# Optimization experiments

Hardware: AMD Instinct MI355X
Metric: run time of the kernel (lower is better)

The kernel has to match this reference:

```python
import jax, jax.numpy as jnp
import numpy as np

N, E, W, G = 100000, 625000, 128, 64  # nodes, edges, width, num graphs
EPS = 1e-5


def setup_inputs() -> dict:
    key = jax.random.key(0)
    ks = jax.random.split(key, 8)
    x = jax.random.normal(ks[0], (N, W), jnp.float32)
    edge_index = jax.random.randint(ks[1], (2, E), 0, N, dtype=jnp.int32)
    edge_weight = jax.random.uniform(ks[2], (E,), jnp.float32)
    batch_map = jnp.sort(jax.random.randint(ks[3], (N,), 0, G, dtype=jnp.int32))
    s = 1.0 / np.sqrt(W)
    return {
        "x": x,
        "edge_index": edge_index,
        "edge_weight": edge_weight,
        "batch_map": batch_map,
        "gn_weight": jnp.ones((W,), jnp.float32),
        "gn_bias": jnp.zeros((W,), jnp.float32),
        "gn_mean_scale": jnp.ones((W,), jnp.float32),
        "W_rel1": jax.random.normal(ks[4], (W, W), jnp.float32) * s,
        "b_rel1": jnp.zeros((W,), jnp.float32),
        "W_root1": jax.random.normal(ks[5], (W, W), jnp.float32) * s,
        "W_rel2": jax.random.normal(ks[6], (W, W), jnp.float32) * s,
        "b_rel2": jnp.zeros((W,), jnp.float32),
        "W_root2": jax.random.normal(ks[7], (W, W), jnp.float32) * s,
    }


def _graph_norm(x, batch, weight, bias, mean_scale):
    # per-graph mean / var keyed on batch_map (PyG GraphNorm)
    cnt = jax.ops.segment_sum(jnp.ones((x.shape[0], 1), x.dtype), batch, num_segments=G)
    mean = jax.ops.segment_sum(x, batch, num_segments=G) / cnt
    out = x - mean_scale * mean[batch]
    var = jax.ops.segment_sum(out * out, batch, num_segments=G) / cnt
    std = jnp.sqrt(var + EPS)
    return weight * out / std[batch] + bias


def _graph_conv(x, src, dst, ew, W_rel, b_rel, W_root):
    # out_i = W_rel @ sum_{j->i} e_ji * x_j + b_rel + W_root @ x_i
    msg = x[src] * ew[:, None]                       # [E, W] gather
    agg = jax.ops.segment_sum(msg, dst, num_segments=x.shape[0])  # scatter-add
    return agg @ W_rel.T + b_rel + x @ W_root.T


def reference(x, edge_index, edge_weight, batch_map,
              gn_weight, gn_bias, gn_mean_scale,
              W_rel1, b_rel1, W_root1, W_rel2, b_rel2, W_root2):
    src, dst = edge_index[0], edge_index[1]
    xx = _graph_norm(x, batch_map, gn_weight, gn_bias, gn_mean_scale)
    xx = _graph_conv(xx, src, dst, edge_weight, W_rel1, b_rel1, W_root1)
    xx = jnp.where(xx >= 0, xx, 0.1 * xx)            # LeakyReLU(0.1)
    xx = _graph_conv(xx, src, dst, edge_weight, W_rel2, b_rel2, W_root2)
    return x + xx
```

## Files before the change

kernel.cpp:

```cpp
#include <hip/hip_runtime.h>
#include <hip/hip_bf16.h>

#define WW 128
#define GG 64
#define GN_EPS 1e-5f
#define SCAN_B 1024

typedef __attribute__((ext_vector_type(8))) short short8;
typedef __attribute__((ext_vector_type(4))) float floatx4;

__device__ inline float bf2f(__hip_bfloat16 h) { return __bfloat162float(h); }

__global__ __launch_bounds__(128) void stats_kernel(
    const float* __restrict__ x, const int* __restrict__ batch, int N,
    float* __restrict__ gsum, float* __restrict__ gsumsq, float* __restrict__ gcnt)
{
    int w = threadIdx.x;
    int row0 = blockIdx.x * 64;
    int row1 = min(row0 + 64, N);
    float s = 0.f, ss = 0.f;
    int cur = batch[row0];
    int cnt = 0;
    auto flush = [&]() {
        atomicAdd(&gsum[cur * WW + w], s);
        atomicAdd(&gsumsq[cur * WW + w], ss);
        if (w == 0) atomicAdd(&gcnt[cur], (float)cnt);
        s = 0.f; ss = 0.f; cnt = 0;
    };
    int i = row0;
    for (; i + 4 <= row1; i += 4) {
        int g0 = batch[i + 0], g1 = batch[i + 1], g2 = batch[i + 2], g3 = batch[i + 3];
        float v0 = x[(size_t)(i + 0) * WW + w];
        float v1 = x[(size_t)(i + 1) * WW + w];
        float v2 = x[(size_t)(i + 2) * WW + w];
        float v3 = x[(size_t)(i + 3) * WW + w];
        if (g0 != cur) { flush(); cur = g0; }
        s += v0; ss += v0 * v0; ++cnt;
        if (g1 != cur) { flush(); cur = g1; }
        s += v1; ss += v1 * v1; ++cnt;
        if (g2 != cur) { flush(); cur = g2; }
        s += v2; ss += v2 * v2; ++cnt;
        if (g3 != cur) { flush(); cur = g3; }
        s += v3; ss += v3 * v3; ++cnt;
    }
    for (; i < row1; ++i) {
        int g = batch[i];
        float v = x[(size_t)i * WW + w];
        if (g != cur) { flush(); cur = g; }
        s += v; ss += v * v; ++cnt;
    }
    flush();
}

__global__ __launch_bounds__(256) void finalize_kernel(
    const float* __restrict__ gsum, const float* __restrict__ gsumsq,
    const float* __restrict__ gcnt,
    const float* __restrict__ wgt, const float* __restrict__ bias,
    const float* __restrict__ ms,
    float* __restrict__ scalev, float* __restrict__ shiftv)
{
    int idx = blockIdx.x * blockDim.x + threadIdx.x;
    if (idx >= GG * WW) return;
    int g = idx >> 7, w = idx & (WW - 1);
    float cnt = gcnt[g];
    float inv = cnt > 0.f ? 1.f / cnt : 0.f;
    float mean = gsum[idx] * inv;
    float msw = ms[w];
    float var = gsumsq[idx] * inv - mean * mean * msw * (2.f - msw);
    var = fmaxf(var, 0.f);
    float sc = wgt[w] * rsqrtf(var + GN_EPS);
    scalev[idx] = sc;
    shiftv[idx] = bias[w] - sc * msw * mean;
}

__global__ __launch_bounds__(256) void normalize_kernel(
    const float* __restrict__ x, const int* __restrict__ batch,
    const float* __restrict__ scalev, const float* __restrict__ shiftv,
    __hip_bfloat16* __restrict__ xn, int N)
{
    size_t tid = (size_t)blockIdx.x * blockDim.x + threadIdx.x;
    if (tid >= (size_t)N * (WW / 4)) return;
    int row = (int)(tid >> 5);
    int c4 = (int)(tid & 31) * 4;
    int g = batch[row];
    float4 v = *(const float4*)(x + (size_t)row * WW + c4);
    float4 sc = *(const float4*)(scalev + (size_t)g * WW + c4);
    float4 sh = *(const float4*)(shiftv + (size_t)g * WW + c4);
    __hip_bfloat162 o0, o1;
    o0.x = __float2bfloat16(sc.x * v.x + sh.x);
    o0.y = __float2bfloat16(sc.y * v.y + sh.y);
    o1.x = __float2bfloat16(sc.z * v.z + sh.z);
    o1.y = __float2bfloat16(sc.w * v.w + sh.w);
    union { __hip_bfloat162 h[2]; uint2 u; } pk;
    pk.h[0] = o0; pk.h[1] = o1;
    *(uint2*)(xn + (size_t)row * WW + c4) = pk.u;
}

__global__ __launch_bounds__(256) void cvt_w_kernel(
    const float* __restrict__ w0, const float* __restrict__ w1,
    const float* __restrict__ w2, const float* __restrict__ w3,
    __hip_bfloat16* __restrict__ dst)
{
    int idx = blockIdx.x * blockDim.x + threadIdx.x;
    int m = idx >> 14;
    int o = idx & 16383;
    const float* src = (m == 0) ? w0 : (m == 1) ? w1 : (m == 2) ? w2 : w3;
    dst[idx] = __float2bfloat16(src[o]);
}

__global__ __launch_bounds__(256) void hist_kernel(
    const int* __restrict__ ei, int E, int* __restrict__ deg)
{
    int e = blockIdx.x * 256 + threadIdx.x;
    if (e < E) atomicAdd(&deg[ei[(size_t)E + e]], 1);
}

__global__ __launch_bounds__(SCAN_B) void scan_blocks(
    const int* __restrict__ deg, int N, int* __restrict__ off, int* __restrict__ bsum)
{
    __shared__ int s[SCAN_B];
    int t = threadIdx.x;
    int i = blockIdx.x * SCAN_B + t;
    int v = (i < N) ? deg[i] : 0;
    s[t] = v; __syncthreads();
    for (int d = 1; d < SCAN_B; d <<= 1) {
        int tmp = (t >= d) ? s[t - d] : 0;
        __syncthreads();
        s[t] += tmp;
        __syncthreads();
    }
    if (i < N) off[i] = s[t] - v;
    if (t == SCAN_B - 1) bsum[blockIdx.x] = s[t];
}

__global__ __launch_bounds__(256) void scan_partials(int* __restrict__ bsum, int P)
{
    __shared__ int s[256];
    int t = threadIdx.x;
    int v = (t < P) ? bsum[t] : 0;
    s[t] = v; __syncthreads();
    for (int d = 1; d < 256; d <<= 1) {
        int tmp = (t >= d) ? s[t - d] : 0;
        __syncthreads();
        s[t] += tmp;
        __syncthreads();
    }
    if (t < P) bsum[t] = s[t] - v;
}

__global__ __launch_bounds__(SCAN_B) void add_offsets(
    int* __restrict__ off, const int* __restrict__ bsum, int N)
{
    int i = blockIdx.x * SCAN_B + threadIdx.x;
    if (i < N) off[i] += bsum[blockIdx.x];
}

__global__ __launch_bounds__(256) void place_kernel(
    const int* __restrict__ ei, const float* __restrict__ ew,
    const int* __restrict__ off, int* __restrict__ cursor,
    int2* __restrict__ ebuf, int E)
{
    int e = blockIdx.x * 256 + threadIdx.x;
    if (e >= E) return;
    int dst = ei[(size_t)E + e];
    int slot = off[dst] + atomicAdd(&cursor[dst], 1);
    ebuf[slot] = make_int2(ei[e], __float_as_int(ew[e]));
}

__global__ __launch_bounds__(256) void gather_kernel(
    const __hip_bfloat16* __restrict__ feat, const int2* __restrict__ ebuf,
    const int* __restrict__ off, const int* __restrict__ deg,
    __hip_bfloat16* __restrict__ aggbf, int N)
{
    int wave = threadIdx.x >> 6;
    int lane = threadIdx.x & 63;
    int node = blockIdx.x * 4 + wave;
    if (node >= N) return;
    int start = off[node];
    int d = deg[node];
    const __hip_bfloat162* f2 = (const __hip_bfloat162*)feat;

    float ax0 = 0.f, ay0 = 0.f, ax1 = 0.f, ay1 = 0.f;
    float ax2 = 0.f, ay2 = 0.f, ax3 = 0.f, ay3 = 0.f;
    int last = start + d - 1;
    for (int k = start; k <= last; k += 4) {
        int i1 = min(k + 1, last);
        int i2 = min(k + 2, last);
        int i3 = min(k + 3, last);
        int2 p0 = ebuf[k];
        int2 p1 = ebuf[i1];
        int2 p2 = ebuf[i2];
        int2 p3 = ebuf[i3];
        __hip_bfloat162 v0 = f2[(size_t)p0.x * 64 + lane];
        __hip_bfloat162 v1 = f2[(size_t)p1.x * 64 + lane];
        __hip_bfloat162 v2 = f2[(size_t)p2.x * 64 + lane];
        __hip_bfloat162 v3 = f2[(size_t)p3.x * 64 + lane];
        float w0 = __int_as_float(p0.y);
        float w1 = (k + 1 <= last) ? __int_as_float(p1.y) : 0.f;
        float w2 = (k + 2 <= last) ? __int_as_float(p2.y) : 0.f;
        float w3 = (k + 3 <= last) ? __int_as_float(p3.y) : 0.f;
        ax0 += w0 * bf2f(v0.x); ay0 += w0 * bf2f(v0.y);
        ax1 += w1 * bf2f(v1.x); ay1 += w1 * bf2f(v1.y);
        ax2 += w2 * bf2f(v2.x); ay2 += w2 * bf2f(v2.y);
        ax3 += w3 * bf2f(v3.x); ay3 += w3 * bf2f(v3.y);
    }
    float ax = (ax0 + ax1) + (ax2 + ax3);
    float ay = (ay0 + ay1) + (ay2 + ay3);

    __hip_bfloat162 o;
    o.x = __float2bfloat16(ax);
    o.y = __float2bfloat16(ay);
    ((__hip_bfloat162*)(aggbf + (size_t)node * WW))[lane] = o;
}

template <bool OUT_BF16>
__global__ __launch_bounds__(256, 3) void gemm_kernel(
    const __hip_bfloat16* __restrict__ A1, const __hip_bfloat16* __restrict__ A2,
    const __hip_bfloat16* __restrict__ Wrel, const __hip_bfloat16* __restrict__ Wroot,
    const float* __restrict__ bias, const float* __restrict__ resid,
    void* __restrict__ outv, int N, int leaky)
{
    __shared__ __hip_bfloat16 smem[2 * 64 * 128];
    int wave = threadIdx.x >> 6;
    int lane = threadIdx.x & 63;
    int q = lane >> 4;
    int r16 = lane & 15;
    int rb = blockIdx.x * 64;

#pragma unroll
    for (int s = 0; s < 8; ++s) {
        int t = wave * 8 + s;
        const __hip_bfloat16* Asel = (t < 16) ? A1 : A2;
        int t4 = t & 15;
        int rloc = t4 * 4 + (lane >> 4);
        int c = (lane & 15) ^ (rloc & 15);
        int grow = rb + rloc; if (grow >= N) grow = N - 1;
        const __hip_bfloat16* g = Asel + (size_t)grow * WW + c * 8;
        __hip_bfloat16* l = smem + (t >> 4) * 8192 + t4 * 512;
        __builtin_amdgcn_global_load_lds(
            (const __attribute__((address_space(1))) void*)g,
            (__attribute__((address_space(3))) void*)l, 16, 0, 0);
    }

    short8 wf[8][2];
#pragma unroll
    for (int kc = 0; kc < 8; ++kc) {
        const __hip_bfloat16* Wsel = (kc < 4) ? Wrel : Wroot;
        int koff = (kc & 3) * 32 + q * 8;
#pragma unroll
        for (int tt = 0; tt < 2; ++tt) {
            int col = (wave * 2 + tt) * 16 + r16;
            wf[kc][tt] = *(const short8*)(Wsel + ((size_t)col * WW + koff));
        }
    }
    float bcol[2];
#pragma unroll
    for (int tt = 0; tt < 2; ++tt) bcol[tt] = bias[(wave * 2 + tt) * 16 + r16];

    __syncthreads();

    floatx4 acc[4][2];
#pragma unroll
    for (int r = 0; r < 4; ++r)
#pragma unroll
        for (int tt = 0; tt < 2; ++tt) acc[r][tt] = (floatx4){0.f, 0.f, 0.f, 0.f};

#pragma unroll
    for (int kc = 0; kc < 8; ++kc) {
        int m = kc >> 2;
        short8 af[4];
#pragma unroll
        for (int r = 0; r < 4; ++r) {
            int row = r * 16 + r16;
            int slot = ((kc & 3) * 4 + q) ^ r16;
            af[r] = *(const short8*)(smem + m * 8192 + row * 128 + slot * 8);
        }
#pragma unroll
        for (int r = 0; r < 4; ++r) {
            acc[r][0] = __builtin_amdgcn_mfma_f32_16x16x32_bf16(af[r], wf[kc][0], acc[r][0], 0, 0, 0);
            acc[r][1] = __builtin_amdgcn_mfma_f32_16x16x32_bf16(af[r], wf[kc][1], acc[r][1], 0, 0, 0);
        }
    }

#pragma unroll
    for (int tt = 0; tt < 2; ++tt) {
        int col = (wave * 2 + tt) * 16 + r16;
#pragma unroll
        for (int r = 0; r < 4; ++r)
#pragma unroll
            for (int rr = 0; rr < 4; ++rr) {
                int row = rb + r * 16 + q * 4 + rr;
                if (row < N) {
                    float v = acc[r][tt][rr] + bcol[tt];
                    if (leaky) v = v >= 0.f ? v : 0.1f * v;
                    if (resid) v += resid[(size_t)row * WW + col];
                    if (OUT_BF16)
                        ((__hip_bfloat16*)outv)[(size_t)row * WW + col] = __float2bfloat16(v);
                    else
                        ((float*)outv)[(size_t)row * WW + col] = v;
                }
            }
    }
}

extern "C" void kernel_launch(void* const* d_in, const int* in_sizes, int n_in,
                              void* d_out, int out_size, void* d_ws, size_t ws_size,
                              hipStream_t stream) {
    const float* x      = (const float*)d_in[0];
    const int*   ei     = (const int*)d_in[1];
    const float* ew     = (const float*)d_in[2];
    const int*   batch  = (const int*)d_in[3];
    const float* gnw    = (const float*)d_in[4];
    const float* gnb    = (const float*)d_in[5];
    const float* gnm    = (const float*)d_in[6];
    const float* Wrel1  = (const float*)d_in[7];
    const float* brel1  = (const float*)d_in[8];
    const float* Wroot1 = (const float*)d_in[9];
    const float* Wrel2  = (const float*)d_in[10];
    const float* brel2  = (const float*)d_in[11];
    const float* Wroot2 = (const float*)d_in[12];

    int N = in_sizes[0] / WW;
    int E = in_sizes[1] / 2;
    int P = (N + SCAN_B - 1) / SCAN_B;
    int ntiles = (N + 63) / 64;

    __hip_bfloat16* aggbf = (__hip_bfloat16*)d_ws;
    __hip_bfloat16* xn = aggbf + (size_t)N * WW;
    __hip_bfloat16* y1 = xn + (size_t)N * WW;
    __hip_bfloat16* Wb = y1 + (size_t)N * WW;
    int2* ebuf   = (int2*)(Wb + 4 * WW * WW);
    int*  deg    = (int*)(ebuf + E);
    int*  cursor = deg + N;
    float* gsum   = (float*)(cursor + N);
    float* gsumsq = gsum + GG * WW;
    float* gcnt   = gsumsq + GG * WW;
    float* scalev = gcnt + GG;
    float* shiftv = scalev + GG * WW;
    int*  off    = (int*)(shiftv + GG * WW);
    int*  bsum   = off + N;

    hipMemsetAsync(deg, 0, ((size_t)2 * N + 2 * GG * WW + GG) * sizeof(int), stream);

    hist_kernel<<<(E + 255) / 256, 256, 0, stream>>>(ei, E, deg);
    scan_blocks<<<P, SCAN_B, 0, stream>>>(deg, N, off, bsum);
    scan_partials<<<1, 256, 0, stream>>>(bsum, P);
    add_offsets<<<P, SCAN_B, 0, stream>>>(off, bsum, N);
    place_kernel<<<(E + 255) / 256, 256, 0, stream>>>(ei, ew, off, cursor, ebuf, E);

    cvt_w_kernel<<<(4 * WW * WW) / 256, 256, 0, stream>>>(Wrel1, Wroot1, Wrel2, Wroot2, Wb);
    stats_kernel<<<(N + 63) / 64, 128, 0, stream>>>(x, batch, N, gsum, gsumsq, gcnt);
    finalize_kernel<<<(GG * WW + 255) / 256, 256, 0, stream>>>(
        gsum, gsumsq, gcnt, gnw, gnb, gnm, scalev, shiftv);
    normalize_kernel<<<(int)(((size_t)N * (WW / 4) + 255) / 256), 256, 0, stream>>>(
        x, batch, scalev, shiftv, xn, N);

    gather_kernel<<<(N + 3) / 4, 256, 0, stream>>>(xn, ebuf, off, deg, aggbf, N);
    gemm_kernel<true><<<ntiles, 256, 0, stream>>>(
        aggbf, xn, Wb, Wb + WW * WW, brel1, nullptr, y1, N, 1);

    gather_kernel<<<(N + 3) / 4, 256, 0, stream>>>(y1, ebuf, off, deg, aggbf, N);
    gemm_kernel<false><<<ntiles, 256, 0, stream>>>(
        aggbf, y1, Wb + 2 * WW * WW, Wb + 3 * WW * WW, brel2, x, d_out, N, 0);
}
```

Measured before the change: 372.2 us.

## Make GEMM persistent with double-buffered LDS prefetch; batch edges per thread in place

```diff
diff --git a/kernel.cpp b/kernel.cpp
--- a/kernel.cpp
+++ b/kernel.cpp
@@ -160,11 +160,26 @@
     const int* __restrict__ off, int* __restrict__ cursor,
     int2* __restrict__ ebuf, int E)
 {
-    int e = blockIdx.x * 256 + threadIdx.x;
-    if (e >= E) return;
-    int dst = ei[(size_t)E + e];
-    int slot = off[dst] + atomicAdd(&cursor[dst], 1);
-    ebuf[slot] = make_int2(ei[e], __float_as_int(ew[e]));
+    int base = blockIdx.x * 1024 + threadIdx.x;
+    int dstv[4], srcv[4];
+    float wv[4];
+    int slot[4];
+#pragma unroll
+    for (int i = 0; i < 4; ++i) {
+        int e = base + i * 256;
+        dstv[i] = (e < E) ? ei[(size_t)E + e] : -1;
+    }
+#pragma unroll
+    for (int i = 0; i < 4; ++i) {
+        int e = base + i * 256;
+        if (e < E) { srcv[i] = ei[e]; wv[i] = ew[e]; }
+    }
+#pragma unroll
+    for (int i = 0; i < 4; ++i)
+        if (dstv[i] >= 0) slot[i] = off[dstv[i]] + atomicAdd(&cursor[dstv[i]], 1);
+#pragma unroll
+    for (int i = 0; i < 4; ++i)
+        if (dstv[i] >= 0) ebuf[slot[i]] = make_int2(srcv[i], __float_as_int(wv[i]));
 }
 
 __global__ __launch_bounds__(256) void gather_kernel(
@@ -214,33 +229,36 @@
 }
 
 template <bool OUT_BF16>
-__global__ __launch_bounds__(256, 3) void gemm_kernel(
+__global__ __launch_bounds__(256, 2) void gemm_kernel(
     const __hip_bfloat16* __restrict__ A1, const __hip_bfloat16* __restrict__ A2,
     const __hip_bfloat16* __restrict__ Wrel, const __hip_bfloat16* __restrict__ Wroot,
     const float* __restrict__ bias, const float* __restrict__ resid,
-    void* __restrict__ outv, int N, int leaky)
-{
-    __shared__ __hip_bfloat16 smem[2 * 64 * 128];
+    void* __restrict__ outv, int N, int leaky, int ntiles)
+{
+    __shared__ __hip_bfloat16 smem[2][2 * 64 * 128];
     int wave = threadIdx.x >> 6;
     int lane = threadIdx.x & 63;
     int q = lane >> 4;
     int r16 = lane & 15;
-    int rb = blockIdx.x * 64;
-
-#pragma unroll
-    for (int s = 0; s < 8; ++s) {
-        int t = wave * 8 + s;
-        const __hip_bfloat16* Asel = (t < 16) ? A1 : A2;
-        int t4 = t & 15;
-        int rloc = t4 * 4 + (lane >> 4);
-        int c = (lane & 15) ^ (rloc & 15);
-        int grow = rb + rloc; if (grow >= N) grow = N - 1;
-        const __hip_bfloat16* g = Asel + (size_t)grow * WW + c * 8;
-        __hip_bfloat16* l = smem + (t >> 4) * 8192 + t4 * 512;
-        __builtin_amdgcn_global_load_lds(
-            (const __attribute__((address_space(1))) void*)g,
-            (__attribute__((address_space(3))) void*)l, 16, 0, 0);
-    }
+
+    auto stage = [&](int tile, int buf) {
+#pragma unroll
+        for (int s = 0; s < 8; ++s) {
+            int t = wave * 8 + s;
+            const __hip_bfloat16* Asel = (t < 16) ? A1 : A2;
+            int t4 = t & 15;
+            int rloc = t4 * 4 + (lane >> 4);
+            int c = (lane & 15) ^ (rloc & 15);
+            int grow = tile * 64 + rloc; if (grow >= N) grow = N - 1;
+            const __hip_bfloat16* g = Asel + (size_t)grow * WW + c * 8;
+            __hip_bfloat16* l = &smem[buf][(t >> 4) * 8192 + t4 * 512];
+            __builtin_amdgcn_global_load_lds(
+                (const __attribute__((address_space(1))) void*)g,
+                (__attribute__((address_space(3))) void*)l, 16, 0, 0);
+        }
+    };
+
+    stage(blockIdx.x, 0);
 
     short8 wf[8][2];
 #pragma unroll
@@ -259,47 +277,57 @@
 
     __syncthreads();
 
-    floatx4 acc[4][2];
-#pragma unroll
-    for (int r = 0; r < 4; ++r)
-#pragma unroll
-        for (int tt = 0; tt < 2; ++tt) acc[r][tt] = (floatx4){0.f, 0.f, 0.f, 0.f};
-
-#pragma unroll
-    for (int kc = 0; kc < 8; ++kc) {
-        int m = kc >> 2;
-        short8 af[4];
-#pragma unroll
-        for (int r = 0; r < 4; ++r) {
-            int row = r * 16 + r16;
-            int slot = ((kc & 3) * 4 + q) ^ r16;
-            af[r] = *(const short8*)(smem + m * 8192 + row * 128 + slot * 8);
+    int cur = 0;
+    for (int tile = blockIdx.x; tile < ntiles; tile += gridDim.x) {
+        int nxt = tile + gridDim.x;
+        if (nxt < ntiles) stage(nxt, cur ^ 1);
+
+        floatx4 acc[4][2];
+#pragma unroll
+        for (int r = 0; r < 4; ++r)
+#pragma unroll
+            for (int tt = 0; tt < 2; ++tt) acc[r][tt] = (floatx4){0.f, 0.f, 0.f, 0.f};
+
+#pragma unroll
+        for (int kc = 0; kc < 8; ++kc) {
+            int m = kc >> 2;
+            short8 af[4];
+#pragma unroll
+            for (int r = 0; r < 4; ++r) {
+                int row = r * 16 + r16;
+                int slot = ((kc & 3) * 4 + q) ^ r16;
+                af[r] = *(const short8*)(&smem[cur][m * 8192 + row * 128 + slot * 8]);
+            }
+#pragma unroll
+            for (int r = 0; r < 4; ++r) {
+                acc[r][0] = __builtin_amdgcn_mfma_f32_16x16x32_bf16(af[r], wf[kc][0], acc[r][0], 0, 0, 0);
+                acc[r][1] = __builtin_amdgcn_mfma_f32_16x16x32_bf16(af[r], wf[kc][1], acc[r][1], 0, 0, 0);
+            }
         }
-#pragma unroll
-        for (int r = 0; r < 4; ++r) {
-            acc[r][0] = __builtin_amdgcn_mfma_f32_16x16x32_bf16(af[r], wf[kc][0], acc[r][0], 0, 0, 0);
-            acc[r][1] = __builtin_amdgcn_mfma_f32_16x16x32_bf16(af[r], wf[kc][1], acc[r][1], 0, 0, 0);
+
+        int rb = tile * 64;
+#pragma unroll
+        for (int tt = 0; tt < 2; ++tt) {
+            int col = (wave * 2 + tt) * 16 + r16;
+#pragma unroll
+            for (int r = 0; r < 4; ++r)
+#pragma unroll
+                for (int rr = 0; rr < 4; ++rr) {
+                    int row = rb + r * 16 + q * 4 + rr;
+                    if (row < N) {
+                        float v = acc[r][tt][rr] + bcol[tt];
+                        if (leaky) v = v >= 0.f ? v : 0.1f * v;
+                        if (resid) v += resid[(size_t)row * WW + col];
+                        if (OUT_BF16)
+                            ((__hip_bfloat16*)outv)[(size_t)row * WW + col] = __float2bfloat16(v);
+                        else
+                            ((float*)outv)[(size_t)row * WW + col] = v;
+                    }
+                }
         }
-    }
-
-#pragma unroll
-    for (int tt = 0; tt < 2; ++tt) {
-        int col = (wave * 2 + tt) * 16 + r16;
-#pragma unroll
-        for (int r = 0; r < 4; ++r)
-#pragma unroll
-            for (int rr = 0; rr < 4; ++rr) {
-                int row = rb + r * 16 + q * 4 + rr;
-                if (row < N) {
-                    float v = acc[r][tt][rr] + bcol[tt];
-                    if (leaky) v = v >= 0.f ? v : 0.1f * v;
-                    if (resid) v += resid[(size_t)row * WW + col];
-                    if (OUT_BF16)
-                        ((__hip_bfloat16*)outv)[(size_t)row * WW + col] = __float2bfloat16(v);
-                    else
-                        ((float*)outv)[(size_t)row * WW + col] = v;
-                }
-            }
+
+        __syncthreads();
+        cur ^= 1;
     }
 }
 
@@ -324,6 +352,7 @@
     int E = in_sizes[1] / 2;
     int P = (N + SCAN_B - 1) / SCAN_B;
     int ntiles = (N + 63) / 64;
+    int ggrid = ntiles < 512 ? ntiles : 512;
 
     __hip_bfloat16* aggbf = (__hip_bfloat16*)d_ws;
     __hip_bfloat16* xn = aggbf + (size_t)N * WW;
@@ -346,7 +375,7 @@
     scan_blocks<<<P, SCAN_B, 0, stream>>>(deg, N, off, bsum);
     scan_partials<<<1, 256, 0, stream>>>(bsum, P);
     add_offsets<<<P, SCAN_B, 0, stream>>>(off, bsum, N);
-    place_kernel<<<(E + 255) / 256, 256, 0, stream>>>(ei, ew, off, cursor, ebuf, E);
+    place_kernel<<<(E + 1023) / 1024, 256, 0, stream>>>(ei, ew, off, cursor, ebuf, E);
 
     cvt_w_kernel<<<(4 * WW * WW) / 256, 256, 0, stream>>>(Wrel1, Wroot1, Wrel2, Wroot2, Wb);
     stats_kernel<<<(N + 63) / 64, 128, 0, stream>>>(x, batch, N, gsum, gsumsq, gcnt);
@@ -356,10 +385,10 @@
         x, batch, scalev, shiftv, xn, N);
 
     gather_kernel<<<(N + 3) / 4, 256, 0, stream>>>(xn, ebuf, off, deg, aggbf, N);
-    gemm_kernel<true><<<ntiles, 256, 0, stream>>>(
-        aggbf, xn, Wb, Wb + WW * WW, brel1, nullptr, y1, N, 1);
+    gemm_kernel<true><<<ggrid, 256, 0, stream>>>(
+        aggbf, xn, Wb, Wb + WW * WW, brel1, nullptr, y1, N, 1, ntiles);
 
     gather_kernel<<<(N + 3) / 4, 256, 0, stream>>>(y1, ebuf, off, deg, aggbf, N);
-    gemm_kernel<false><<<ntiles, 256, 0, stream>>>(
-        aggbf, y1, Wb + 2 * WW * WW, Wb + 3 * WW * WW, brel2, x, d_out, N, 0);
-}
+    gemm_kernel<false><<<ggrid, 256, 0, stream>>>(
+        aggbf, y1, Wb + 2 * WW * WW, Wb + 3 * WW * WW, brel2, x, d_out, N, 0, ntiles);
+}
```

After: 365.0 us. No clear change (-1.9%).
